# Kernel optimization log

Measured on AMD Instinct MI355X. Metric: run time of the kernel, lower is better.

The kernel has to match this reference:

```python
import jax, jax.numpy as jnp
import numpy as np

RPN_BBOX_STD_DEV = np.array([0.1, 0.1, 0.2, 0.2], np.float32)
PRE_NMS_LIMIT = 6000
PROPOSAL_COUNTS = 1000
NMS_THRESHOLD = 0.7
B, N = 8, 262144


def setup_inputs() -> dict:
    key = jax.random.key(0)
    k1, k2, k3, k4 = jax.random.split(key, 4)
    # rpn_class: softmax probs over {bg, fg}
    rpn_class = jax.nn.softmax(jax.random.normal(k1, (B, N, 2), dtype=jnp.float32), axis=-1)
    # rpn_bbox: small refinement deltas (pre std-dev scaling)
    rpn_bbox = jax.random.normal(k2, (B, N, 4), dtype=jnp.float32) * 0.5
    # anchors: valid normalized boxes (y1,x1,y2,x2) in [0,1]
    cy = jax.random.uniform(k3, (B, N), minval=0.05, maxval=0.95)
    cx = jax.random.uniform(jax.random.fold_in(k3, 1), (B, N), minval=0.05, maxval=0.95)
    h = jax.random.uniform(k4, (B, N), minval=0.02, maxval=0.3)
    w = jax.random.uniform(jax.random.fold_in(k4, 1), (B, N), minval=0.02, maxval=0.3)
    anchors = jnp.stack([cy - h / 2, cx - w / 2, cy + h / 2, cx + w / 2], axis=-1)
    return {"rpn_class": rpn_class, "rpn_bbox": rpn_bbox, "anchors": anchors}


def apply_box_deltas(boxes, deltas):
    # boxes, deltas: [..., 4] in (y1, x1, y2, x2) / (dy, dx, log dh, log dw)
    h = boxes[..., 2] - boxes[..., 0]
    w = boxes[..., 3] - boxes[..., 1]
    cy = boxes[..., 0] + 0.5 * h
    cx = boxes[..., 1] + 0.5 * w
    cy = cy + deltas[..., 0] * h
    cx = cx + deltas[..., 1] * w
    h = h * jnp.exp(deltas[..., 2])
    w = w * jnp.exp(deltas[..., 3])
    return jnp.stack([cy - 0.5 * h, cx - 0.5 * w, cy + 0.5 * h, cx + 0.5 * w], axis=-1)


def clip_boxes(boxes):
    # clip to normalized window [0, 0, 1, 1]
    return jnp.clip(boxes, 0.0, 1.0)


def _iou_one_vs_all(box, boxes):
    y1 = jnp.maximum(box[0], boxes[:, 0])
    x1 = jnp.maximum(box[1], boxes[:, 1])
    y2 = jnp.minimum(box[2], boxes[:, 2])
    x2 = jnp.minimum(box[3], boxes[:, 3])
    inter = jnp.maximum(y2 - y1, 0.0) * jnp.maximum(x2 - x1, 0.0)
    area1 = (box[2] - box[0]) * (box[3] - box[1])
    areas = (boxes[:, 2] - boxes[:, 0]) * (boxes[:, 3] - boxes[:, 1])
    return inter / (area1 + areas - inter + 1e-9)


def nms_pad(boxes, scores, iou_thr, max_out):
    # boxes: [K, 4], scores: [K]. Greedy NMS, zero-padded to max_out (as tf NMS + pad).
    NEG = jnp.float32(-1e9)
    k = boxes.shape[0]
    arange = jnp.arange(k)

    def step(scores_rem, _):
        idx = jnp.argmax(scores_rem)
        valid = scores_rem[idx] > NEG * 0.5
        iou = _iou_one_vs_all(boxes[idx], boxes)
        suppress = (iou > iou_thr) | (arange == idx)
        scores_new = jnp.where(suppress, NEG, scores_rem)
        return scores_new, (idx, valid)

    _, (idxs, valids) = jax.lax.scan(step, scores, None, length=max_out)
    proposals = boxes[idxs] * valids[:, None].astype(boxes.dtype)  # zero-pad invalid
    return proposals


def reference(rpn_class, rpn_bbox, anchors):
    # scores: foreground class probability
    scores = rpn_class[:, :, 1]                                    # [B, N]
    deltas = rpn_bbox * jnp.asarray(RPN_BBOX_STD_DEV).reshape(1, 1, 4)
    pre_nms_limit = min(PRE_NMS_LIMIT, anchors.shape[1])
    top_scores, ix = jax.lax.top_k(scores, pre_nms_limit)          # [B, K]
    deltas_k = jnp.take_along_axis(deltas, ix[..., None], axis=1)  # [B, K, 4]
    anchors_k = jnp.take_along_axis(anchors, ix[..., None], axis=1)
    boxes = clip_boxes(apply_box_deltas(anchors_k, deltas_k))      # [B, K, 4]
    proposals = jax.vmap(lambda b, s: nms_pad(b, s, NMS_THRESHOLD, PROPOSAL_COUNTS))(boxes, top_scores)
    return proposals                                               # [B, PROPOSAL_COUNTS, 4]
```

## Files before the change

### kernel.cpp

```cpp
#include <hip/hip_runtime.h>
#include <cstdint>
#include <math.h>

#define NBATCH 8
#define NANCH 262144
#define TOPK 6000
#define OUTK 1000
#define CAP 16384
#define ROWS 6016
#define MROWS 2048
#define MWORDS 32
#define NT2 528
#define NBIN 8192

using u32 = uint32_t;
using u64 = unsigned long long;

__device__ inline u32 binof(u64 key, u32 m) {
    u32 hb  = (u32)(key >> 52);
    u32 mid = (u32)(key >> 41) & 0x7FFu;
    u32 bi = (hb - m) * 2048u + mid;
    return bi > (NBIN - 1) ? (NBIN - 1) : bi;
}

__global__ void hist_kernel(const float* __restrict__ cls, u32* __restrict__ hist,
                            u32* __restrict__ hist16) {
    __shared__ u32 lh[4096];
    int b = blockIdx.y, t = threadIdx.x;
    for (int i = blockIdx.x * 256 + t; i < NBIN; i += gridDim.x * 256)
        hist16[(size_t)b * NBIN + i] = 0;
    for (int i = t; i < 4096; i += 256) lh[i] = 0;
    __syncthreads();
    const float4* p4 = (const float4*)(cls + (size_t)b * NANCH * 2);
    const int P = NANCH / 2;
    for (int p = blockIdx.x * 256 + t; p < P; p += gridDim.x * 256) {
        float4 v = p4[p];
        atomicAdd(&lh[__float_as_uint(v.y) >> 20], 1);
        atomicAdd(&lh[__float_as_uint(v.w) >> 20], 1);
    }
    __syncthreads();
    for (int i = t; i < 4096; i += 256) { u32 c = lh[i]; if (c) atomicAdd(&hist[b * 4096 + i], c); }
}

__global__ void compact_kernel(const float* __restrict__ cls, const u32* __restrict__ hist,
                               u32* __restrict__ meta, u64* __restrict__ cand,
                               u32* __restrict__ hist16) {
    __shared__ u64 buf[4096];
    __shared__ u32 ts[256];
    __shared__ u32 thr, lc, gbase;
    int b = blockIdx.y, t = threadIdx.x;
    if (t == 0) lc = 0;
    const u32* h = hist + b * 4096;
    u32 s = 0;
    for (int k = 0; k < 16; k++) s += h[t * 16 + k];
    ts[t] = s; __syncthreads();
    u32 suf = 0;
    for (int t2 = t + 1; t2 < 256; t2++) suf += ts[t2];
    if (suf < TOPK && suf + s >= TOPK) {
        u32 a = suf;
        for (int k = 15; k >= 0; k--) {
            u32 c = h[t * 16 + k];
            if (a + c >= TOPK) { thr = (u32)(t * 16 + k) << 20; break; }
            a += c;
        }
    }
    __syncthreads();
    u32 T = thr;
    if (t == 0) meta[56 + b] = T >> 20;
    const float4* p4 = (const float4*)(cls + (size_t)b * NANCH * 2);
    const int P = NANCH / 2;
    for (int p = blockIdx.x * 256 + t; p < P; p += gridDim.x * 256) {
        float4 v = p4[p];
        u32 k0 = __float_as_uint(v.y), k1 = __float_as_uint(v.w);
        u32 n0 = 2u * (u32)p, n1 = n0 + 1u;
        if (k0 >= T) { u32 q = atomicAdd(&lc, 1u); buf[q] = ((u64)k0 << 32) | (u32)(~n0); }
        if (k1 >= T) { u32 q = atomicAdd(&lc, 1u); buf[q] = ((u64)k1 << 32) | (u32)(~n1); }
    }
    __syncthreads();
    if (t == 0) gbase = atomicAdd(&meta[48 + b], lc);
    __syncthreads();
    u32 base = gbase, n = lc, m = T >> 20;
    u32* h16 = hist16 + (size_t)b * NBIN;
    for (u32 j = t; j < n; j += 256) {
        u32 d = base + j;
        if (d < CAP) {
            u64 key = buf[j];
            cand[(size_t)b * CAP + d] = key;
            atomicAdd(&h16[binof(key, m)], 1u);
        }
    }
}

__global__ __launch_bounds__(256) void scan_kernel(u32* __restrict__ hist16) {
    __shared__ u32 part[256];
    int b = blockIdx.x, t = threadIdx.x;
    u32* h = hist16 + (size_t)b * NBIN;
    u32 s = 0;
    for (int k = 0; k < 32; k++) s += h[t * 32 + k];
    part[t] = s; __syncthreads();
    u32 suf = 0;
    for (int t2 = t + 1; t2 < 256; t2++) suf += part[t2];
    u32 cur = suf;
    for (int k = 31; k >= 0; k--) {
        u32 c = h[t * 32 + k];
        h[t * 32 + k] = cur;
        cur += c;
    }
}

__global__ __launch_bounds__(256) void scatter_kernel(const u64* __restrict__ cand,
                                                      const u32* __restrict__ meta,
                                                      u32* __restrict__ hist16,
                                                      u64* __restrict__ grouped) {
    int b = blockIdx.y;
    int i = blockIdx.x * 256 + threadIdx.x;
    u32 cnt = meta[48 + b]; if (cnt > CAP) cnt = CAP;
    if (i >= (int)cnt) return;
    u32 m = meta[56 + b];
    u64 key = cand[(size_t)b * CAP + i];
    u32 bi = binof(key, m);
    u32 p = atomicAdd(&hist16[(size_t)b * NBIN + bi], 1u);
    if (p < CAP) grouped[(size_t)b * CAP + p] = key;
}

__global__ __launch_bounds__(256) void rank_kernel(
                            const u64* __restrict__ grouped, const u32* __restrict__ meta,
                            const float* __restrict__ anchors, const float* __restrict__ bbox,
                            float4* __restrict__ boxes, float* __restrict__ areas) {
    int b = blockIdx.y, t = threadIdx.x;
    int p = blockIdx.x * 256 + t;
    u32 cnt = meta[48 + b]; if (cnt > CAP) cnt = CAP;
    if (blockIdx.x == 0 && t < ROWS - TOPK) {
        boxes[(size_t)b * ROWS + TOPK + t] = make_float4(0.f, 0.f, 0.f, 0.f);
        areas[(size_t)b * ROWS + TOPK + t] = 0.f;
    }
    if (p >= (int)cnt) return;
    u32 m = meta[56 + b];
    const u64* gb = grouped + (size_t)b * CAP;
    u64 key = gb[p];
    u32 bi = binof(key, m);
    int s = p;
    while (s > 0 && binof(gb[s - 1], m) == bi) s--;
    u32 r = 0;
    int q = s;
    while (q < (int)cnt) {
        u64 kq = gb[q];
        if (binof(kq, m) != bi) break;
        r += (kq > key) ? 1u : 0u;
        q++;
    }
    u32 rank = (u32)s + r;
    if (rank < TOPK) {
        u32 idx = ~(u32)(key & 0xFFFFFFFFull);
        size_t off = ((size_t)b * NANCH + idx) * 4;
        const float4 a = *(const float4*)(anchors + off);
        const float4 d = *(const float4*)(bbox + off);
        float h = a.z - a.x, w = a.w - a.y;
        float cy = a.x + 0.5f * h, cx = a.y + 0.5f * w;
        float dy = d.x * 0.1f, dx = d.y * 0.1f, dh = d.z * 0.2f, dw = d.w * 0.2f;
        cy = cy + dy * h; cx = cx + dx * w;
        h = h * (float)exp((double)dh);
        w = w * (float)exp((double)dw);
        float y1 = cy - 0.5f * h, x1 = cx - 0.5f * w;
        float y2 = cy + 0.5f * h, x2 = cx + 0.5f * w;
        y1 = fminf(fmaxf(y1, 0.f), 1.f); x1 = fminf(fmaxf(x1, 0.f), 1.f);
        y2 = fminf(fmaxf(y2, 0.f), 1.f); x2 = fminf(fmaxf(x2, 0.f), 1.f);
        boxes[(size_t)b * ROWS + rank] = make_float4(y1, x1, y2, x2);
        areas[(size_t)b * ROWS + rank] = (y2 - y1) * (x2 - x1);
    }
}

__device__ inline u64 readlane64(u64 x, int sl) {
    u32 lo = (u32)__builtin_amdgcn_readlane((int)(u32)x, sl);
    u32 hi = (u32)__builtin_amdgcn_readlane((int)(u32)(x >> 32), sl);
    return ((u64)hi << 32) | lo;
}
__device__ inline u64 wave_or64(u64 x) {
    u32 lo = (u32)x, hi = (u32)(x >> 32);
    lo |= __builtin_amdgcn_ds_swizzle(lo, 0x041F); hi |= __builtin_amdgcn_ds_swizzle(hi, 0x041F);
    lo |= __builtin_amdgcn_ds_swizzle(lo, 0x081F); hi |= __builtin_amdgcn_ds_swizzle(hi, 0x081F);
    lo |= __builtin_amdgcn_ds_swizzle(lo, 0x101F); hi |= __builtin_amdgcn_ds_swizzle(hi, 0x101F);
    lo |= __builtin_amdgcn_ds_swizzle(lo, 0x201F); hi |= __builtin_amdgcn_ds_swizzle(hi, 0x201F);
    lo |= __builtin_amdgcn_ds_swizzle(lo, 0x401F); hi |= __builtin_amdgcn_ds_swizzle(hi, 0x401F);
    u32 l0 = (u32)__builtin_amdgcn_readlane((int)lo, 0)  | (u32)__builtin_amdgcn_readlane((int)lo, 32);
    u32 h0 = (u32)__builtin_amdgcn_readlane((int)hi, 0)  | (u32)__builtin_amdgcn_readlane((int)hi, 32);
    return ((u64)h0 << 32) | l0;
}

__global__ __launch_bounds__(256) void nms_mask_kernel(const float4* __restrict__ boxes,
                                                       const float* __restrict__ areas,
                                                       u64* __restrict__ Mt) {
    const float  EPS  = 3.8146972656e-06f;
    const double MIDD = (double)0.7f + 2.9802322387695312e-08;
    __shared__ float4 scol[4][64];
    __shared__ float  sare[4][64];
    int b = blockIdx.y;
    int wv = threadIdx.x >> 6, l = threadIdx.x & 63;
    int tid = blockIdx.x * 4 + wv;
    if (tid >= NT2) return;
    int cb = (int)((sqrt(8.0 * (double)tid + 1.0) - 1.0) * 0.5);
    while ((cb + 1) * (cb + 2) / 2 <= tid) cb++;
    while (cb * (cb + 1) / 2 > tid) cb--;
    int rt = tid - cb * (cb + 1) / 2;
    const float4* bx = boxes + (size_t)b * ROWS;
    const float*  ar = areas + (size_t)b * ROWS;
    scol[wv][l] = bx[cb * 64 + l];
    sare[wv][l] = ar[cb * 64 + l];
    int row = rt * 64 + l;
    float4 r4 = bx[row];
    float  rar = ar[row];
    u32 wlo = 0, whi = 0; u64 unc = 0;
    #pragma unroll
    for (int c = 63; c >= 0; c--) {
        float4 c4 = scol[wv][c];
        float  caf = sare[wv][c];
        float y1 = fmaxf(r4.x, c4.x), x1 = fmaxf(r4.y, c4.y);
        float y2 = fminf(r4.z, c4.z), x2 = fminf(r4.w, c4.w);
        float inter = fmaxf(y2 - y1, 0.f) * fmaxf(x2 - x1, 0.f);
        float uni = ((rar + caf) - inter) + 1e-9f;
        float d = fmaf(uni, -0.7f, inter);
        float tt = uni * EPS;
        u32 sup = (d > tt) ? 1u : 0u;
        unc |= __ballot(fabsf(d) <= tt);
        if (c >= 32) whi = (whi << 1) | sup;
        else         wlo = (wlo << 1) | sup;
    }
    if (unc) {
        wlo = 0; whi = 0;
        for (int c = 63; c >= 0; c--) {
            float4 c4 = scol[wv][c]; float caf = sare[wv][c];
            float y1 = fmaxf(r4.x, c4.x), x1 = fmaxf(r4.y, c4.y);
            float y2 = fminf(r4.z, c4.z), x2 = fminf(r4.w, c4.w);
            float inter = fmaxf(y2 - y1, 0.f) * fmaxf(x2 - x1, 0.f);
            float uni = ((rar + caf) - inter) + 1e-9f;
            double td = fma((double)uni, -MIDD, (double)inter);
            u32 sup = (td >= 0.0) ? 1u : 0u;
            if (c >= 32) whi = (whi << 1) | sup;
            else         wlo = (wlo << 1) | sup;
        }
    }
    u64 w = ((u64)whi << 32) | wlo;
    if (cb == rt) {
        w &= (l < 63) ? (~0ull << (l + 1)) : 0ull;
        u64 tw = 0;
        for (int c2 = 0; c2 < 64; c2++) {
            u64 bc = __ballot((u32)((w >> c2) & 1ull) != 0u);
            if (l == c2) tw = bc;
        }
        w = tw | (1ull << l);
    }
    Mt[((size_t)b * MWORDS + cb) * MROWS + row] = w;
}

__global__ __launch_bounds__(64) void nms_seq_kernel(const float4* __restrict__ boxes,
                                                     const float* __restrict__ areas,
                                                     const u64* __restrict__ Mt,
                                                     float* __restrict__ out) {
    const double MIDD = (double)0.7f + 2.9802322387695312e-08;
    __shared__ u32 keptIdx[1024];
    __shared__ float4 sbox[1024];
    __shared__ float  skar[1024];
    int b = blockIdx.x, l = threadIdx.x;
    const u64* Mb = Mt + (size_t)b * MWORDS * MROWS;
    const float4* bx = boxes + (size_t)b * ROWS;
    const float*  ar = areas + (size_t)b * ROWS;
    float4* ob = (float4*)(out + (size_t)b * OUTK * 4);
    const u64 below = (1ull << l) - 1ull;
    int kept = 0;
    u64 rw = 0;
    u64 dw0 = Mb[l];
    float4 vb0 = bx[l];  float va0 = ar[l];
    u64 X0 = Mb[(size_t)MROWS + l];
    u64 dw1 = Mb[(size_t)MROWS + 64 + l];
    float4 vb1 = bx[64 + l]; float va1 = ar[64 + l];
    u64 X1 = Mb[(size_t)2 * MROWS + 64 + l];
    u64 gp = 0;
    for (int c = 0; c < MWORDS; c++) {
        int base = c * 64;
        u64 alive = ~rw;
        u64 K = alive;
        while (true) {
            u64 Kn = alive & ~__ballot((dw0 & K & below) != 0ull);
            if (Kn == K) break;
            K = Kn;
        }
        int avail = OUTK - kept;
        int nk  = (int)__popcll(K);
        int pos = (int)__popcll(K & below);
        u32 keptme = (u32)((K >> l) & 1ull);
        if (nk > avail) keptme &= (u32)(pos < avail);
        if (keptme) {
            int opos = kept + pos;
            ob[opos] = vb0;
            keptIdx[opos] = (u32)(base + l);
            sbox[opos] = vb0;
            skar[opos] = va0;
        }
        kept += (nk < avail) ? nk : avail;
        if (kept >= OUTK || c + 1 >= MWORDS) break;
        rw = wave_or64((keptme ? X0 : 0ull) | gp);
        __syncthreads();
        u64 dw2 = 0, X2 = 0; float4 vb2 = make_float4(0.f, 0.f, 0.f, 0.f); float va2 = 0.f;
        u64 gpn = 0;
        if (c + 2 < MWORDS) {
            int nb2 = base + 128;
            dw2 = Mb[(size_t)(c + 2) * MROWS + nb2 + l];
            vb2 = bx[nb2 + l]; va2 = ar[nb2 + l];
            if (c + 3 < MWORDS) X2 = Mb[(size_t)(c + 3) * MROWS + nb2 + l];
            int K2g = kept;
            if (K2g > 0) {
                #pragma unroll
                for (int u = 0; u < 16; u++) {
                    int k = l + (u << 6);
                    u32 idx = keptIdx[(k < K2g) ? k : K2g - 1];
                    gpn |= Mb[(size_t)(c + 2) * MROWS + idx];
                }
            }
        }
        dw0 = dw1; X0 = X1; vb0 = vb1; va0 = va1;
        dw1 = dw2; X1 = X2; vb1 = vb2; va1 = va2;
        gp = gpn;
    }
    if (kept < OUTK) {
        __syncthreads();
        for (int i = MROWS; i < TOPK && kept < OUTK; i++) {
            float4 c4 = bx[i]; float ca = ar[i];
            int sup = 0;
            for (int j = l; j < kept; j += 64) {
                float4 kb = sbox[j]; float ka = skar[j];
                float y1 = fmaxf(kb.x, c4.x), x1 = fmaxf(kb.y, c4.y);
                float y2 = fminf(kb.z, c4.z), x2 = fminf(kb.w, c4.w);
                float inter = fmaxf(y2 - y1, 0.f) * fmaxf(x2 - x1, 0.f);
                float uni = ((ka + ca) - inter) + 1e-9f;
                double td = fma((double)uni, -MIDD, (double)inter);
                sup |= (td >= 0.0) ? 1 : 0;
            }
            if (!__any(sup)) {
                if (l == 0) { ob[kept] = c4; sbox[kept] = c4; skar[kept] = ca; }
                kept++;
            }
        }
    }
    for (int p = kept + l; p < OUTK; p += 64)
        ob[p] = make_float4(0.f, 0.f, 0.f, 0.f);
}

extern "C" void kernel_launch(void* const* d_in, const int* in_sizes, int n_in,
                              void* d_out, int out_size, void* d_ws, size_t ws_size,
                              hipStream_t stream) {
    const float* cls     = (const float*)d_in[0];
    const float* bbox    = (const float*)d_in[1];
    const float* anchors = (const float*)d_in[2];

    char* ws = (char*)d_ws;
    u32* hist1 = (u32*)(ws);
    u32* meta  = (u32*)(ws + 131072);
    float4* boxes = (float4*)(ws + 131328);
    float* areas  = (float*)(ws + 901376);
    u64* Mt = (u64*)(ws + 1093888);
    u32* hist16  = (u32*)(ws + 1093888);
    u64* cand    = (u64*)(ws + 1093888 + 262144);
    u64* grouped = (u64*)(ws + 1093888 + 1310720);
    size_t need = 1093888 + (size_t)NBATCH * MWORDS * MROWS * 8;
    if (ws_size < need) return;

    hipMemsetAsync(ws, 0, 131328, stream);

    hist_kernel<<<dim3(64, NBATCH), 256, 0, stream>>>(cls, hist1, hist16);
    compact_kernel<<<dim3(64, NBATCH), 256, 0, stream>>>(cls, hist1, meta, cand, hist16);
    scan_kernel<<<NBATCH, 256, 0, stream>>>(hist16);
    scatter_kernel<<<dim3(CAP / 256, NBATCH), 256, 0, stream>>>(cand, meta, hist16, grouped);
    rank_kernel<<<dim3(CAP / 256, NBATCH), 256, 0, stream>>>(grouped, meta, anchors, bbox, boxes, areas);
    nms_mask_kernel<<<dim3((NT2 + 3) / 4, NBATCH), 256, 0, stream>>>(boxes, areas, Mt);
    nms_seq_kernel<<<NBATCH, 64, 0, stream>>>(boxes, areas, Mt, (float*)d_out);
}
```

Baseline: 188.3 us.

## Fuse secondary histogram, scan, scatter and rank into one per-batch block kernel

The fine-bin histogram, prefix scan, scatter into grouped order, and per-element rank/box decode are merged into a single 1024-thread kernel per batch that keeps the histogram in shared memory. This removes three kernel launches, the global hist16 buffer and its zeroing, and global atomics. In exchange only 8 blocks do the rank and decode work, where before it was spread over many blocks, so parallelism for that phase drops. The grouped writes go to global memory and are read back after a block-level fence and barrier.

Result: slower. 228.2 us (+21.2%).

```diff
diff --git a/kernel.cpp b/kernel.cpp
--- a/kernel.cpp
+++ b/kernel.cpp
@@ -23,12 +23,9 @@
     return bi > (NBIN - 1) ? (NBIN - 1) : bi;
 }
 
-__global__ void hist_kernel(const float* __restrict__ cls, u32* __restrict__ hist,
-                            u32* __restrict__ hist16) {
+__global__ void hist_kernel(const float* __restrict__ cls, u32* __restrict__ hist) {
     __shared__ u32 lh[4096];
     int b = blockIdx.y, t = threadIdx.x;
-    for (int i = blockIdx.x * 256 + t; i < NBIN; i += gridDim.x * 256)
-        hist16[(size_t)b * NBIN + i] = 0;
     for (int i = t; i < 4096; i += 256) lh[i] = 0;
     __syncthreads();
     const float4* p4 = (const float4*)(cls + (size_t)b * NANCH * 2);
@@ -43,8 +40,7 @@
 }
 
 __global__ void compact_kernel(const float* __restrict__ cls, const u32* __restrict__ hist,
-                               u32* __restrict__ meta, u64* __restrict__ cand,
-                               u32* __restrict__ hist16) {
+                               u32* __restrict__ meta, u64* __restrict__ cand) {
     __shared__ u64 buf[4096];
     __shared__ u32 ts[256];
     __shared__ u32 thr, lc, gbase;
@@ -79,102 +75,96 @@
     __syncthreads();
     if (t == 0) gbase = atomicAdd(&meta[48 + b], lc);
     __syncthreads();
-    u32 base = gbase, n = lc, m = T >> 20;
-    u32* h16 = hist16 + (size_t)b * NBIN;
+    u32 base = gbase, n = lc;
     for (u32 j = t; j < n; j += 256) {
         u32 d = base + j;
-        if (d < CAP) {
-            u64 key = buf[j];
-            cand[(size_t)b * CAP + d] = key;
-            atomicAdd(&h16[binof(key, m)], 1u);
-        }
-    }
-}
-
-__global__ __launch_bounds__(256) void scan_kernel(u32* __restrict__ hist16) {
-    __shared__ u32 part[256];
+        if (d < CAP) cand[(size_t)b * CAP + d] = buf[j];
+    }
+}
+
+__global__ __launch_bounds__(1024) void group_rank_kernel(
+                            const u64* __restrict__ cand, const u32* __restrict__ meta,
+                            const float* __restrict__ anchors, const float* __restrict__ bbox,
+                            u64* __restrict__ grouped,
+                            float4* __restrict__ boxes, float* __restrict__ areas) {
+    __shared__ u32 lh[NBIN];
+    __shared__ u32 part[1024];
+    __shared__ u32 wsum[16];
     int b = blockIdx.x, t = threadIdx.x;
-    u32* h = hist16 + (size_t)b * NBIN;
-    u32 s = 0;
-    for (int k = 0; k < 32; k++) s += h[t * 32 + k];
-    part[t] = s; __syncthreads();
-    u32 suf = 0;
-    for (int t2 = t + 1; t2 < 256; t2++) suf += part[t2];
-    u32 cur = suf;
-    for (int k = 31; k >= 0; k--) {
-        u32 c = h[t * 32 + k];
-        h[t * 32 + k] = cur;
-        cur += c;
-    }
-}
-
-__global__ __launch_bounds__(256) void scatter_kernel(const u64* __restrict__ cand,
-                                                      const u32* __restrict__ meta,
-                                                      u32* __restrict__ hist16,
-                                                      u64* __restrict__ grouped) {
-    int b = blockIdx.y;
-    int i = blockIdx.x * 256 + threadIdx.x;
+    int wv = t >> 6, l = t & 63;
     u32 cnt = meta[48 + b]; if (cnt > CAP) cnt = CAP;
-    if (i >= (int)cnt) return;
     u32 m = meta[56 + b];
-    u64 key = cand[(size_t)b * CAP + i];
-    u32 bi = binof(key, m);
-    u32 p = atomicAdd(&hist16[(size_t)b * NBIN + bi], 1u);
-    if (p < CAP) grouped[(size_t)b * CAP + p] = key;
-}
-
-__global__ __launch_bounds__(256) void rank_kernel(
-                            const u64* __restrict__ grouped, const u32* __restrict__ meta,
-                            const float* __restrict__ anchors, const float* __restrict__ bbox,
-                            float4* __restrict__ boxes, float* __restrict__ areas) {
-    int b = blockIdx.y, t = threadIdx.x;
-    int p = blockIdx.x * 256 + t;
-    u32 cnt = meta[48 + b]; if (cnt > CAP) cnt = CAP;
-    if (blockIdx.x == 0 && t < ROWS - TOPK) {
+    const u64* cb = cand + (size_t)b * CAP;
+    u64* gb = grouped + (size_t)b * CAP;
+    if (t < ROWS - TOPK) {
         boxes[(size_t)b * ROWS + TOPK + t] = make_float4(0.f, 0.f, 0.f, 0.f);
         areas[(size_t)b * ROWS + TOPK + t] = 0.f;
     }
-    if (p >= (int)cnt) return;
-    u32 m = meta[56 + b];
-    const u64* gb = grouped + (size_t)b * CAP;
-    u64 key = gb[p];
-    u32 bi = binof(key, m);
-    int s = p;
-    while (s > 0 && binof(gb[s - 1], m) == bi) s--;
-    u32 r = 0;
-    int q = s;
-    while (q < (int)cnt) {
-        u64 kq = gb[q];
-        if (binof(kq, m) != bi) break;
-        r += (kq > key) ? 1u : 0u;
-        q++;
-    }
-    u32 rank = (u32)s + r;
-    if (rank < TOPK) {
-        u32 idx = ~(u32)(key & 0xFFFFFFFFull);
-        size_t off = ((size_t)b * NANCH + idx) * 4;
-        const float4 a = *(const float4*)(anchors + off);
-        const float4 d = *(const float4*)(bbox + off);
-        float h = a.z - a.x, w = a.w - a.y;
-        float cy = a.x + 0.5f * h, cx = a.y + 0.5f * w;
-        float dy = d.x * 0.1f, dx = d.y * 0.1f, dh = d.z * 0.2f, dw = d.w * 0.2f;
-        cy = cy + dy * h; cx = cx + dx * w;
-        h = h * (float)exp((double)dh);
-        w = w * (float)exp((double)dw);
-        float y1 = cy - 0.5f * h, x1 = cx - 0.5f * w;
-        float y2 = cy + 0.5f * h, x2 = cx + 0.5f * w;
-        y1 = fminf(fmaxf(y1, 0.f), 1.f); x1 = fminf(fmaxf(x1, 0.f), 1.f);
-        y2 = fminf(fmaxf(y2, 0.f), 1.f); x2 = fminf(fmaxf(x2, 0.f), 1.f);
-        boxes[(size_t)b * ROWS + rank] = make_float4(y1, x1, y2, x2);
-        areas[(size_t)b * ROWS + rank] = (y2 - y1) * (x2 - x1);
-    }
-}
-
-__device__ inline u64 readlane64(u64 x, int sl) {
-    u32 lo = (u32)__builtin_amdgcn_readlane((int)(u32)x, sl);
-    u32 hi = (u32)__builtin_amdgcn_readlane((int)(u32)(x >> 32), sl);
-    return ((u64)hi << 32) | lo;
-}
+    #pragma unroll
+    for (int k = 0; k < NBIN / 1024; k++) lh[t + k * 1024] = 0;
+    __syncthreads();
+    for (u32 i = t; i < cnt; i += 1024) atomicAdd(&lh[binof(cb[i], m)], 1u);
+    __syncthreads();
+    u32 s = 0;
+    #pragma unroll
+    for (int k = 0; k < 8; k++) s += lh[t * 8 + k];
+    part[t] = s;
+    __syncthreads();
+    u32 wsuf = 0;
+    for (int k = l + 1; k < 64; k++) wsuf += part[(wv << 6) + k];
+    if (l == 0) wsum[wv] = wsuf + part[wv << 6];
+    __syncthreads();
+    u32 cur = wsuf;
+    for (int k = wv + 1; k < 16; k++) cur += wsum[k];
+    #pragma unroll
+    for (int k = 7; k >= 0; k--) {
+        u32 c = lh[t * 8 + k];
+        lh[t * 8 + k] = cur;
+        cur += c;
+    }
+    __syncthreads();
+    for (u32 i = t; i < cnt; i += 1024) {
+        u64 key = cb[i];
+        u32 p = atomicAdd(&lh[binof(key, m)], 1u);
+        if (p < CAP) gb[p] = key;
+    }
+    __threadfence_block();
+    __syncthreads();
+    for (u32 pi = t; pi < cnt; pi += 1024) {
+        u64 key = gb[pi];
+        u32 bi = binof(key, m);
+        int sp = (int)pi;
+        while (sp > 0 && binof(gb[sp - 1], m) == bi) sp--;
+        u32 r = 0;
+        int q = sp;
+        while (q < (int)cnt) {
+            u64 kq = gb[q];
+            if (binof(kq, m) != bi) break;
+            r += (kq > key) ? 1u : 0u;
+            q++;
+        }
+        u32 rank = (u32)sp + r;
+        if (rank < TOPK) {
+            u32 idx = ~(u32)(key & 0xFFFFFFFFull);
+            size_t off = ((size_t)b * NANCH + idx) * 4;
+            const float4 a = *(const float4*)(anchors + off);
+            const float4 d = *(const float4*)(bbox + off);
+            float h = a.z - a.x, w = a.w - a.y;
+            float cy = a.x + 0.5f * h, cx = a.y + 0.5f * w;
+            float dy = d.x * 0.1f, dx = d.y * 0.1f, dh = d.z * 0.2f, dw = d.w * 0.2f;
+            cy = cy + dy * h; cx = cx + dx * w;
+            h = h * (float)exp((double)dh);
+            w = w * (float)exp((double)dw);
+            float y1 = cy - 0.5f * h, x1 = cx - 0.5f * w;
+            float y2 = cy + 0.5f * h, x2 = cx + 0.5f * w;
+            y1 = fminf(fmaxf(y1, 0.f), 1.f); x1 = fminf(fmaxf(x1, 0.f), 1.f);
+            y2 = fminf(fmaxf(y2, 0.f), 1.f); x2 = fminf(fmaxf(x2, 0.f), 1.f);
+            boxes[(size_t)b * ROWS + rank] = make_float4(y1, x1, y2, x2);
+            areas[(size_t)b * ROWS + rank] = (y2 - y1) * (x2 - x1);
+        }
+    }
+}
+
 __device__ inline u64 wave_or64(u64 x) {
     u32 lo = (u32)x, hi = (u32)(x >> 32);
     lo |= __builtin_amdgcn_ds_swizzle(lo, 0x041F); hi |= __builtin_amdgcn_ds_swizzle(hi, 0x041F);
@@ -358,19 +348,16 @@
     float4* boxes = (float4*)(ws + 131328);
     float* areas  = (float*)(ws + 901376);
     u64* Mt = (u64*)(ws + 1093888);
-    u32* hist16  = (u32*)(ws + 1093888);
-    u64* cand    = (u64*)(ws + 1093888 + 262144);
-    u64* grouped = (u64*)(ws + 1093888 + 1310720);
+    u64* cand    = (u64*)(ws + 1093888);
+    u64* grouped = (u64*)(ws + 1093888 + 1048576);
     size_t need = 1093888 + (size_t)NBATCH * MWORDS * MROWS * 8;
     if (ws_size < need) return;
 
     hipMemsetAsync(ws, 0, 131328, stream);
 
-    hist_kernel<<<dim3(64, NBATCH), 256, 0, stream>>>(cls, hist1, hist16);
-    compact_kernel<<<dim3(64, NBATCH), 256, 0, stream>>>(cls, hist1, meta, cand, hist16);
-    scan_kernel<<<NBATCH, 256, 0, stream>>>(hist16);
-    scatter_kernel<<<dim3(CAP / 256, NBATCH), 256, 0, stream>>>(cand, meta, hist16, grouped);
-    rank_kernel<<<dim3(CAP / 256, NBATCH), 256, 0, stream>>>(grouped, meta, anchors, bbox, boxes, areas);
+    hist_kernel<<<dim3(64, NBATCH), 256, 0, stream>>>(cls, hist1);
+    compact_kernel<<<dim3(64, NBATCH), 256, 0, stream>>>(cls, hist1, meta, cand);
+    group_rank_kernel<<<NBATCH, 1024, 0, stream>>>(cand, meta, anchors, bbox, grouped, boxes, areas);
     nms_mask_kernel<<<dim3((NT2 + 3) / 4, NBATCH), 256, 0, stream>>>(boxes, areas, Mt);
     nms_seq_kernel<<<NBATCH, 64, 0, stream>>>(boxes, areas, Mt, (float*)d_out);
 }
```
